# Performance work log

Hardware: AMD Instinct MI355X
Metric: run time of the kernel (lower is better)

## Reference

```python
import jax, jax.numpy as jnp
import numpy as np

HEADS = 8  # head_count from init_kwargs

def _conv1x1(x, W, b):
    # x: [B,C,H,W], W: [Cout,Cin], b: [Cout] -> [B,Cout,H,W]
    return jnp.einsum('bchw,kc->bkhw', x, W) + b[None, :, None, None]

def setup_inputs() -> dict:
    key = jax.random.key(0)
    ks = jax.random.split(key, 9)
    B, C, H, W = 16, 128, 128, 128
    KC, VC = 128, 128
    s = 0.05
    return {
        'x':  jax.random.normal(ks[0], (B, C, H, W), dtype=jnp.float32),
        'Wk': jax.random.normal(ks[1], (KC, C), dtype=jnp.float32) * s,
        'bk': jnp.zeros((KC,), dtype=jnp.float32),
        'Wq': jax.random.normal(ks[2], (KC, C), dtype=jnp.float32) * s,
        'bq': jnp.zeros((KC,), dtype=jnp.float32),
        'Wv': jax.random.normal(ks[3], (VC, C), dtype=jnp.float32) * s,
        'bv': jnp.zeros((VC,), dtype=jnp.float32),
        'Wr': jax.random.normal(ks[4], (C, VC), dtype=jnp.float32) * s,
        'br': jnp.zeros((C,), dtype=jnp.float32),
    }

def reference(x, Wk, bk, Wq, bq, Wv, bv, Wr, br):
    B, C, H, W = x.shape
    N = H * W
    KC, VC = Wk.shape[0], Wv.shape[0]
    dk, dv = KC // HEADS, VC // HEADS

    keys = _conv1x1(x, Wk, bk).reshape(B, HEADS, dk, N)
    queries = _conv1x1(x, Wq, bq).reshape(B, HEADS, dk, N)
    values = _conv1x1(x, Wv, bv).reshape(B, HEADS, dv, N)

    k = jax.nn.softmax(keys, axis=-1)      # softmax over spatial positions
    q = jax.nn.softmax(queries, axis=2)    # softmax over per-head key channels

    # context: [B,h,dk,dv] = sum_n k[b,h,k,n] * v[b,h,v,n]
    context = jnp.einsum('bhkn,bhvn->bhkv', k, values)
    # attended: [B,h,dv,N] = context^T @ q
    attended = jnp.einsum('bhkv,bhkn->bhvn', context, q)
    aggregated = attended.reshape(B, VC, H, W)

    reprojected = _conv1x1(aggregated, Wr, br)
    return reprojected + x
```

## Files before the change

kernel.cpp:

```cpp
#include <hip/hip_runtime.h>
#include <hip/hip_bf16.h>

#define BATCH 16
#define CH    128
#define NPIX  16384
#define NHEAD 8

typedef __attribute__((ext_vector_type(8))) short bf16x8;
typedef __attribute__((ext_vector_type(4))) float f32x4;

__device__ __forceinline__ short f2b(float f) {
    union { float f; unsigned u; } v; v.f = f;
    unsigned r = v.u + 0x7fffu + ((v.u >> 16) & 1u);
    return (short)(r >> 16);
}
__device__ __forceinline__ float b2f(ushort u) {
    union { unsigned u; float f; } v; v.u = ((unsigned)u) << 16; return v.f;
}

__device__ __forceinline__ int xswz(int p, int c) {
    const int v = ((p >> 2) & 15) ^ ((p & 3) << 2);
    return (p * CH + c) ^ (v << 3);
}

__global__ __launch_bounds__(256)
void k1_context(const float* __restrict__ x,
                const float* __restrict__ Wk, const float* __restrict__ bk,
                const float* __restrict__ Wv, const float* __restrict__ bv,
                float* __restrict__ Sp, float* __restrict__ Zp)
{
    __shared__ __align__(16) ushort xlds[64 * CH];

    const int tid  = threadIdx.x;
    const int w    = tid >> 6;
    const int lane = tid & 63;
    const int lo   = lane & 15;
    const int hi   = lane >> 4;

    const int b     = blockIdx.x >> 6;
    const int chunk = blockIdx.x & 63;
    const float* xb = x + (size_t)b * CH * NPIX;

    const int pc = tid >> 4;
    const int pL = tid & 15;

    float4 pf[8];
    {
        const int p0 = chunk * 256;
        #pragma unroll
        for (int i = 0; i < 8; ++i)
            pf[i] = *(const float4*)(xb + (size_t)(pc + 16*i) * NPIX + p0 + pL * 4);
    }

    bf16x8 wkf[2][4], wvf[2][4];
    #pragma unroll
    for (int ct = 0; ct < 2; ++ct) {
        const int row = 32*w + ct*16 + lo;
        #pragma unroll
        for (int ks = 0; ks < 4; ++ks) {
            const int c0 = ks*32 + hi*8;
            const float4 k0 = *(const float4*)(Wk + row*CH + c0);
            const float4 k1 = *(const float4*)(Wk + row*CH + c0 + 4);
            const float4 v0 = *(const float4*)(Wv + row*CH + c0);
            const float4 v1 = *(const float4*)(Wv + row*CH + c0 + 4);
            bf16x8 fk, fv;
            fk[0]=f2b(k0.x); fk[1]=f2b(k0.y); fk[2]=f2b(k0.z); fk[3]=f2b(k0.w);
            fk[4]=f2b(k1.x); fk[5]=f2b(k1.y); fk[6]=f2b(k1.z); fk[7]=f2b(k1.w);
            fv[0]=f2b(v0.x); fv[1]=f2b(v0.y); fv[2]=f2b(v0.z); fv[3]=f2b(v0.w);
            fv[4]=f2b(v1.x); fv[5]=f2b(v1.y); fv[6]=f2b(v1.z); fv[7]=f2b(v1.w);
            wkf[ct][ks] = fk; wvf[ct][ks] = fv;
        }
    }
    float bkv[2], bvv[2];
    #pragma unroll
    for (int ct = 0; ct < 2; ++ct) {
        bkv[ct] = bk[32*w + ct*16 + lo];
        bvv[ct] = bv[32*w + ct*16 + lo];
    }

    const f32x4 zero4 = {0.f, 0.f, 0.f, 0.f};
    f32x4 sacc[2] = {zero4, zero4};
    float zacc[2] = {0.f, 0.f};

    #pragma unroll
    for (int sub = 0; sub < 4; ++sub) {
        #pragma unroll
        for (int i = 0; i < 8; ++i) {
            const int c = pc + 16*i;
            #pragma unroll
            for (int kk = 0; kk < 4; ++kk)
                xlds[xswz(pL*4 + kk, c)] = (ushort)f2b(((const float*)&pf[i])[kk]);
        }
        __syncthreads();

        if (sub < 3) {
            const int pn = chunk*256 + (sub+1)*64;
            #pragma unroll
            for (int i = 0; i < 8; ++i)
                pf[i] = *(const float4*)(xb + (size_t)(pc + 16*i) * NPIX + pn + pL * 4);
        }

        #pragma unroll
        for (int ct = 0; ct < 2; ++ct) {
            f32x4 dk_[4], dv_[4];
            #pragma unroll
            for (int pt = 0; pt < 4; ++pt) { dk_[pt] = zero4; dv_[pt] = zero4; }
            #pragma unroll
            for (int ks = 0; ks < 4; ++ks) {
                #pragma unroll
                for (int pt = 0; pt < 4; ++pt) {
                    const bf16x8 xa = *(const bf16x8*)&xlds[xswz(pt*16 + lo, ks*32 + hi*8)];
                    dk_[pt] = __builtin_amdgcn_mfma_f32_16x16x32_bf16(xa, wkf[ct][ks], dk_[pt], 0, 0, 0);
                    dv_[pt] = __builtin_amdgcn_mfma_f32_16x16x32_bf16(xa, wvf[ct][ks], dv_[pt], 0, 0, 0);
                }
            }
            bf16x8 ef[2], vf[2];
            #pragma unroll
            for (int pt = 0; pt < 4; ++pt) {
                #pragma unroll
                for (int r = 0; r < 4; ++r) {
                    float e = __expf(dk_[pt][r] + bkv[ct]);
                    zacc[ct] += e;
                    ef[pt >> 1][(pt & 1)*4 + r] = f2b(e);
                    vf[pt >> 1][(pt & 1)*4 + r] = f2b(dv_[pt][r] + bvv[ct]);
                }
            }
            #pragma unroll
            for (int kg = 0; kg < 2; ++kg)
                sacc[ct] = __builtin_amdgcn_mfma_f32_16x16x32_bf16(ef[kg], vf[kg], sacc[ct], 0, 0, 0);
        }
        __syncthreads();
    }

    float* sp = Sp + (size_t)(b*64 + chunk) * 2048;
    #pragma unroll
    for (int ct = 0; ct < 2; ++ct)
        #pragma unroll
        for (int r = 0; r < 4; ++r)
            sp[(2*w + ct)*256 + (hi*4 + r)*16 + lo] = sacc[ct][r];

    #pragma unroll
    for (int ct = 0; ct < 2; ++ct) {
        float z = zacc[ct];
        z += __shfl_xor(z, 16, 64);
        z += __shfl_xor(z, 32, 64);
        if (hi == 0)
            Zp[(size_t)(b*64 + chunk) * 128 + 32*w + ct*16 + lo] = z;
    }
}

__global__ __launch_bounds__(256)
void k1b_reduce(const float* __restrict__ Sp, const float* __restrict__ Zp,
                float* __restrict__ Sg, float* __restrict__ Zg)
{
    const int b = blockIdx.y;
    const int j = blockIdx.x * 256 + threadIdx.x;
    if (j < 2048) {
        const float* p = Sp + (size_t)b * 64 * 2048 + j;
        float a = 0.f;
        #pragma unroll 8
        for (int c = 0; c < 64; ++c) a += p[(size_t)c * 2048];
        Sg[b*2048 + j] = a;
    } else if (j < 2176) {
        const int k = j - 2048;
        const float* p = Zp + (size_t)b * 64 * 128 + k;
        float a = 0.f;
        #pragma unroll 8
        for (int c = 0; c < 64; ++c) a += p[(size_t)c * 128];
        Zg[b*128 + k] = a;
    }
}

__global__ __launch_bounds__(256)
void k15_meff(const float* __restrict__ Sg, const float* __restrict__ Zg,
              const float* __restrict__ Wr, ushort* __restrict__ Meffh)
{
    const int b   = blockIdx.x >> 6;
    const int idx = (blockIdx.x & 63) * 256 + threadIdx.x;
    const int c   = idx >> 7;
    const int kcg = idx & 127;
    const int h   = kcg >> 4;
    const int kc  = kcg & 15;
    const float* sp = Sg + (size_t)b*2048 + h*256 + kc*16;
    const float* wr = Wr + (size_t)c * CH + h*16;
    float acc = 0.f;
    #pragma unroll
    for (int v4i = 0; v4i < 4; ++v4i) {
        const float4 sv = *(const float4*)(sp + v4i*4);
        const float4 wv = *(const float4*)(wr + v4i*4);
        acc += sv.x*wv.x + sv.y*wv.y + sv.z*wv.z + sv.w*wv.w;
    }
    Meffh[((size_t)b*CH + c)*CH + kcg] = (ushort)f2b(acc / Zg[b*128 + kcg]);
}

__global__ __launch_bounds__(256)
void k2_out(const float* __restrict__ x,
            const float* __restrict__ Wq, const float* __restrict__ bq,
            const ushort* __restrict__ Meffh, const float* __restrict__ br,
            float* __restrict__ out)
{
    __shared__ __align__(16) ushort xlds[64 * CH];
    __shared__ __align__(16) ushort qlds[64 * CH];
    __shared__ __align__(16) ushort ylds[64 * CH];

    const int tid  = threadIdx.x;
    const int w    = tid >> 6;
    const int lane = tid & 63;
    const int lo   = lane & 15;
    const int hi   = lane >> 4;

    const int b     = blockIdx.x >> 6;
    const int chunk = blockIdx.x & 63;
    const size_t xbase = (size_t)b * CH * NPIX;
    const float* xb = x + xbase;
    float* outb = out + xbase;

    const int pc = tid >> 4;
    const int pL = tid & 15;

    float4 pf[8];
    {
        const int p0 = chunk * 256;
        #pragma unroll
        for (int i = 0; i < 8; ++i)
            pf[i] = *(const float4*)(xb + (size_t)(pc + 16*i) * NPIX + p0 + pL * 4);
    }

    bf16x8 wqf[2][4], mf[2][4];
    #pragma unroll
    for (int ct = 0; ct < 2; ++ct) {
        const int row = 32*w + ct*16 + lo;
        #pragma unroll
        for (int ks = 0; ks < 4; ++ks) {
            const int c0 = ks*32 + hi*8;
            const float4 q0 = *(const float4*)(Wq + row*CH + c0);
            const float4 q1 = *(const float4*)(Wq + row*CH + c0 + 4);
            bf16x8 fq;
            fq[0]=f2b(q0.x); fq[1]=f2b(q0.y); fq[2]=f2b(q0.z); fq[3]=f2b(q0.w);
            fq[4]=f2b(q1.x); fq[5]=f2b(q1.y); fq[6]=f2b(q1.z); fq[7]=f2b(q1.w);
            wqf[ct][ks] = fq;
            mf[ct][ks] = *(const bf16x8*)(Meffh + ((size_t)b*CH + row)*CH + c0);
        }
    }
    float bqv[2];
    #pragma unroll
    for (int ct = 0; ct < 2; ++ct) bqv[ct] = bq[32*w + ct*16 + lo];
    float brv2[8];
    #pragma unroll
    for (int i = 0; i < 8; ++i) brv2[i] = br[pc + 16*i];

    const f32x4 zero4 = {0.f, 0.f, 0.f, 0.f};

    #pragma unroll
    for (int sub = 0; sub < 4; ++sub) {
        const int p0 = chunk*256 + sub*64;

        #pragma unroll
        for (int i = 0; i < 8; ++i) {
            const int c = pc + 16*i;
            #pragma unroll
            for (int kk = 0; kk < 4; ++kk)
                xlds[xswz(pL*4 + kk, c)] = (ushort)f2b(((const float*)&pf[i])[kk]);
        }
        __syncthreads();

        if (sub < 3) {
            const int pn = chunk*256 + (sub+1)*64;
            #pragma unroll
            for (int i = 0; i < 8; ++i)
                pf[i] = *(const float4*)(xb + (size_t)(pc + 16*i) * NPIX + pn + pL * 4);
        }

        f32x4 dq[2][4];
        #pragma unroll
        for (int ct = 0; ct < 2; ++ct)
            #pragma unroll
            for (int pt = 0; pt < 4; ++pt) dq[ct][pt] = zero4;
        #pragma unroll
        for (int ks = 0; ks < 4; ++ks) {
            #pragma unroll
            for (int pt = 0; pt < 4; ++pt) {
                const bf16x8 xa = *(const bf16x8*)&xlds[xswz(pt*16 + lo, ks*32 + hi*8)];
                #pragma unroll
                for (int ct = 0; ct < 2; ++ct)
                    dq[ct][pt] = __builtin_amdgcn_mfma_f32_16x16x32_bf16(xa, wqf[ct][ks], dq[ct][pt], 0, 0, 0);
            }
        }

        #pragma unroll
        for (int ct = 0; ct < 2; ++ct) {
            const int qc = 32*w + ct*16 + lo;
            #pragma unroll
            for (int pt = 0; pt < 4; ++pt) {
                #pragma unroll
                for (int r = 0; r < 4; ++r) {
                    const float e = __expf(dq[ct][pt][r] + bqv[ct]);
                    float s = e;
                    s += __shfl_xor(s, 1, 64);
                    s += __shfl_xor(s, 2, 64);
                    s += __shfl_xor(s, 4, 64);
                    s += __shfl_xor(s, 8, 64);
                    const float q = e / s;
                    const int pos = pt*16 + hi*4 + r;
                    const int sidx = (pos*CH + qc) ^ ((pos & 7) << 3);
                    qlds[sidx] = (ushort)f2b(q);
                }
            }
        }
        __syncthreads();

        f32x4 d2[2][4];
        #pragma unroll
        for (int ct = 0; ct < 2; ++ct)
            #pragma unroll
            for (int pt = 0; pt < 4; ++pt) d2[ct][pt] = zero4;
        #pragma unroll
        for (int ks = 0; ks < 4; ++ks) {
            #pragma unroll
            for (int pt = 0; pt < 4; ++pt) {
                const int pos  = pt*16 + lo;
                const int sidx = (pos*CH + ks*32 + hi*8) ^ ((pos & 7) << 3);
                const bf16x8 qf = *(const bf16x8*)&qlds[sidx];
                #pragma unroll
                for (int ct = 0; ct < 2; ++ct)
                    d2[ct][pt] = __builtin_amdgcn_mfma_f32_16x16x32_bf16(mf[ct][ks], qf, d2[ct][pt], 0, 0, 0);
            }
        }

        #pragma unroll
        for (int ct = 0; ct < 2; ++ct)
            #pragma unroll
            for (int pt = 0; pt < 4; ++pt) {
                #pragma unroll
                for (int r = 0; r < 4; ++r) {
                    const int c = 32*w + ct*16 + hi*4 + r;
                    const int e = c*64 + ((pt*16 + lo) ^ ((c & 7) << 3));
                    ylds[e] = (ushort)f2b(d2[ct][pt][r]);
                }
            }
        __syncthreads();

        #pragma unroll
        for (int i = 0; i < 8; ++i) {
            const int c = pc + 16*i;
            const size_t g = (size_t)c * NPIX + p0 + pL * 4;
            const float4 x4 = *(const float4*)(xb + g);
            const ushort4 y4 = *(const ushort4*)&ylds[c*64 + 4*(pL ^ ((c & 7) << 1))];
            float4 o;
            o.x = b2f(y4.x) + brv2[i] + x4.x;
            o.y = b2f(y4.y) + brv2[i] + x4.y;
            o.z = b2f(y4.z) + brv2[i] + x4.z;
            o.w = b2f(y4.w) + brv2[i] + x4.w;
            *(float4*)(outb + g) = o;
        }
    }
}

extern "C" void kernel_launch(void* const* d_in, const int* in_sizes, int n_in,
                              void* d_out, int out_size, void* d_ws, size_t ws_size,
                              hipStream_t stream)
{
    const float* x  = (const float*)d_in[0];
    const float* Wk = (const float*)d_in[1];
    const float* bk = (const float*)d_in[2];
    const float* Wq = (const float*)d_in[3];
    const float* bq = (const float*)d_in[4];
    const float* Wv = (const float*)d_in[5];
    const float* bv = (const float*)d_in[6];
    const float* Wr = (const float*)d_in[7];
    const float* br = (const float*)d_in[8];
    float* out = (float*)d_out;

    float*  Sp    = (float*)d_ws;
    float*  Zp    = Sp + (size_t)16*64*2048;
    float*  Sg    = Zp + (size_t)16*64*128;
    float*  Zg    = Sg + 32768;
    ushort* Meffh = (ushort*)(Zg + 2048);

    k1_context<<<dim3(BATCH * 64), dim3(256), 0, stream>>>(x, Wk, bk, Wv, bv, Sp, Zp);
    k1b_reduce<<<dim3(9, BATCH),   dim3(256), 0, stream>>>(Sp, Zp, Sg, Zg);
    k15_meff  <<<dim3(BATCH * 64), dim3(256), 0, stream>>>(Sg, Zg, Wr, Meffh);
    k2_out    <<<dim3(BATCH * 64), dim3(256), 0, stream>>>(x, Wq, bq, Meffh, br, out);
}
```

Before: 436.1 us.

## Halve per-block pixel chunk, double-buffer LDS, write output directly without staging

Doubles the grid for the context and output kernels by giving each block 128 pixels instead of 256, which raises parallelism and latency hiding. The context kernel uses a double-buffered LDS tile and drops the trailing barrier. The output kernel removes the ylds staging buffer and its barrier, writing results directly with the residual read back from the bf16 x tile in LDS. This uses a bf16-rounded residual and scalar strided stores, and it also swaps the division for a reciprocal. The cost is more partial sums for the reduce kernel and less-coalesced output stores.

```diff
diff --git a/kernel.cpp b/kernel.cpp
--- a/kernel.cpp
+++ b/kernel.cpp
@@ -29,7 +29,7 @@
                 const float* __restrict__ Wv, const float* __restrict__ bv,
                 float* __restrict__ Sp, float* __restrict__ Zp)
 {
-    __shared__ __align__(16) ushort xlds[64 * CH];
+    __shared__ __align__(16) ushort xlds[2][64 * CH];
 
     const int tid  = threadIdx.x;
     const int w    = tid >> 6;
@@ -37,8 +37,8 @@
     const int lo   = lane & 15;
     const int hi   = lane >> 4;
 
-    const int b     = blockIdx.x >> 6;
-    const int chunk = blockIdx.x & 63;
+    const int b     = blockIdx.x >> 7;
+    const int chunk = blockIdx.x & 127;
     const float* xb = x + (size_t)b * CH * NPIX;
 
     const int pc = tid >> 4;
@@ -46,7 +46,7 @@
 
     float4 pf[8];
     {
-        const int p0 = chunk * 256;
+        const int p0 = chunk * 128;
         #pragma unroll
         for (int i = 0; i < 8; ++i)
             pf[i] = *(const float4*)(xb + (size_t)(pc + 16*i) * NPIX + p0 + pL * 4);
@@ -83,18 +83,21 @@
     float zacc[2] = {0.f, 0.f};
 
     #pragma unroll
-    for (int sub = 0; sub < 4; ++sub) {
-        #pragma unroll
-        for (int i = 0; i < 8; ++i) {
-            const int c = pc + 16*i;
-            #pragma unroll
-            for (int kk = 0; kk < 4; ++kk)
-                xlds[xswz(pL*4 + kk, c)] = (ushort)f2b(((const float*)&pf[i])[kk]);
+    for (int sub = 0; sub < 2; ++sub) {
+        ushort* buf = &xlds[sub][0];
+        if (sub == 0) {
+            #pragma unroll
+            for (int i = 0; i < 8; ++i) {
+                const int c = pc + 16*i;
+                #pragma unroll
+                for (int kk = 0; kk < 4; ++kk)
+                    buf[xswz(pL*4 + kk, c)] = (ushort)f2b(((const float*)&pf[i])[kk]);
+            }
         }
         __syncthreads();
 
-        if (sub < 3) {
-            const int pn = chunk*256 + (sub+1)*64;
+        if (sub == 0) {
+            const int pn = chunk*128 + 64;
             #pragma unroll
             for (int i = 0; i < 8; ++i)
                 pf[i] = *(const float4*)(xb + (size_t)(pc + 16*i) * NPIX + pn + pL * 4);
@@ -109,7 +112,7 @@
             for (int ks = 0; ks < 4; ++ks) {
                 #pragma unroll
                 for (int pt = 0; pt < 4; ++pt) {
-                    const bf16x8 xa = *(const bf16x8*)&xlds[xswz(pt*16 + lo, ks*32 + hi*8)];
+                    const bf16x8 xa = *(const bf16x8*)&buf[xswz(pt*16 + lo, ks*32 + hi*8)];
                     dk_[pt] = __builtin_amdgcn_mfma_f32_16x16x32_bf16(xa, wkf[ct][ks], dk_[pt], 0, 0, 0);
                     dv_[pt] = __builtin_amdgcn_mfma_f32_16x16x32_bf16(xa, wvf[ct][ks], dv_[pt], 0, 0, 0);
                 }
@@ -129,10 +132,20 @@
             for (int kg = 0; kg < 2; ++kg)
                 sacc[ct] = __builtin_amdgcn_mfma_f32_16x16x32_bf16(ef[kg], vf[kg], sacc[ct], 0, 0, 0);
         }
-        __syncthreads();
-    }
-
-    float* sp = Sp + (size_t)(b*64 + chunk) * 2048;
+
+        if (sub == 0) {
+            ushort* nb = &xlds[1][0];
+            #pragma unroll
+            for (int i = 0; i < 8; ++i) {
+                const int c = pc + 16*i;
+                #pragma unroll
+                for (int kk = 0; kk < 4; ++kk)
+                    nb[xswz(pL*4 + kk, c)] = (ushort)f2b(((const float*)&pf[i])[kk]);
+            }
+        }
+    }
+
+    float* sp = Sp + (size_t)(b*128 + chunk) * 2048;
     #pragma unroll
     for (int ct = 0; ct < 2; ++ct)
         #pragma unroll
@@ -145,7 +158,7 @@
         z += __shfl_xor(z, 16, 64);
         z += __shfl_xor(z, 32, 64);
         if (hi == 0)
-            Zp[(size_t)(b*64 + chunk) * 128 + 32*w + ct*16 + lo] = z;
+            Zp[(size_t)(b*128 + chunk) * 128 + 32*w + ct*16 + lo] = z;
     }
 }
 
@@ -156,17 +169,17 @@
     const int b = blockIdx.y;
     const int j = blockIdx.x * 256 + threadIdx.x;
     if (j < 2048) {
-        const float* p = Sp + (size_t)b * 64 * 2048 + j;
+        const float* p = Sp + (size_t)b * 128 * 2048 + j;
         float a = 0.f;
         #pragma unroll 8
-        for (int c = 0; c < 64; ++c) a += p[(size_t)c * 2048];
+        for (int c = 0; c < 128; ++c) a += p[(size_t)c * 2048];
         Sg[b*2048 + j] = a;
     } else if (j < 2176) {
         const int k = j - 2048;
-        const float* p = Zp + (size_t)b * 64 * 128 + k;
+        const float* p = Zp + (size_t)b * 128 * 128 + k;
         float a = 0.f;
         #pragma unroll 8
-        for (int c = 0; c < 64; ++c) a += p[(size_t)c * 128];
+        for (int c = 0; c < 128; ++c) a += p[(size_t)c * 128];
         Zg[b*128 + k] = a;
     }
 }
@@ -201,7 +214,6 @@
 {
     __shared__ __align__(16) ushort xlds[64 * CH];
     __shared__ __align__(16) ushort qlds[64 * CH];
-    __shared__ __align__(16) ushort ylds[64 * CH];
 
     const int tid  = threadIdx.x;
     const int w    = tid >> 6;
@@ -209,8 +221,8 @@
     const int lo   = lane & 15;
     const int hi   = lane >> 4;
 
-    const int b     = blockIdx.x >> 6;
-    const int chunk = blockIdx.x & 63;
+    const int b     = blockIdx.x >> 7;
+    const int chunk = blockIdx.x & 127;
     const size_t xbase = (size_t)b * CH * NPIX;
     const float* xb = x + xbase;
     float* outb = out + xbase;
@@ -220,7 +232,7 @@
 
     float4 pf[8];
     {
-        const int p0 = chunk * 256;
+        const int p0 = chunk * 128;
         #pragma unroll
         for (int i = 0; i < 8; ++i)
             pf[i] = *(const float4*)(xb + (size_t)(pc + 16*i) * NPIX + p0 + pL * 4);
@@ -245,15 +257,17 @@
     float bqv[2];
     #pragma unroll
     for (int ct = 0; ct < 2; ++ct) bqv[ct] = bq[32*w + ct*16 + lo];
-    float brv2[8];
-    #pragma unroll
-    for (int i = 0; i < 8; ++i) brv2[i] = br[pc + 16*i];
+    float brv[2][4];
+    #pragma unroll
+    for (int ct = 0; ct < 2; ++ct)
+        #pragma unroll
+        for (int r = 0; r < 4; ++r) brv[ct][r] = br[32*w + ct*16 + hi*4 + r];
 
     const f32x4 zero4 = {0.f, 0.f, 0.f, 0.f};
 
     #pragma unroll
-    for (int sub = 0; sub < 4; ++sub) {
-        const int p0 = chunk*256 + sub*64;
+    for (int sub = 0; sub < 2; ++sub) {
+        const int p0 = chunk*128 + sub*64;
 
         #pragma unroll
         for (int i = 0; i < 8; ++i) {
@@ -264,8 +278,8 @@
         }
         __syncthreads();
 
-        if (sub < 3) {
-            const int pn = chunk*256 + (sub+1)*64;
+        if (sub == 0) {
+            const int pn = chunk*128 + 64;
             #pragma unroll
             for (int i = 0; i < 8; ++i)
                 pf[i] = *(const float4*)(xb + (size_t)(pc + 16*i) * NPIX + pn + pL * 4);
@@ -300,7 +314,7 @@
                     s += __shfl_xor(s, 2, 64);
                     s += __shfl_xor(s, 4, 64);
                     s += __shfl_xor(s, 8, 64);
-                    const float q = e / s;
+                    const float q = e * __builtin_amdgcn_rcpf(s);
                     const int pos = pt*16 + hi*4 + r;
                     const int sidx = (pos*CH + qc) ^ ((pos & 7) << 3);
                     qlds[sidx] = (ushort)f2b(q);
@@ -331,28 +345,17 @@
         for (int ct = 0; ct < 2; ++ct)
             #pragma unroll
             for (int pt = 0; pt < 4; ++pt) {
+                const int n   = p0 + pt*16 + lo;
+                const int pos = pt*16 + lo;
                 #pragma unroll
                 for (int r = 0; r < 4; ++r) {
-                    const int c = 32*w + ct*16 + hi*4 + r;
-                    const int e = c*64 + ((pt*16 + lo) ^ ((c & 7) << 3));
-                    ylds[e] = (ushort)f2b(d2[ct][pt][r]);
+                    const int cc = 32*w + ct*16 + hi*4 + r;
+                    outb[(size_t)cc * NPIX + n] =
+                        d2[ct][pt][r] + brv[ct][r] + b2f(xlds[xswz(pos, cc)]);
                 }
             }
-        __syncthreads();
-
-        #pragma unroll
-        for (int i = 0; i < 8; ++i) {
-            const int c = pc + 16*i;
-            const size_t g = (size_t)c * NPIX + p0 + pL * 4;
-            const float4 x4 = *(const float4*)(xb + g);
-            const ushort4 y4 = *(const ushort4*)&ylds[c*64 + 4*(pL ^ ((c & 7) << 1))];
-            float4 o;
-            o.x = b2f(y4.x) + brv2[i] + x4.x;
-            o.y = b2f(y4.y) + brv2[i] + x4.y;
-            o.z = b2f(y4.z) + brv2[i] + x4.z;
-            o.w = b2f(y4.w) + brv2[i] + x4.w;
-            *(float4*)(outb + g) = o;
-        }
+
+        if (sub == 0) __syncthreads();
     }
 }
 
@@ -372,13 +375,13 @@
     float* out = (float*)d_out;
 
     float*  Sp    = (float*)d_ws;
-    float*  Zp    = Sp + (size_t)16*64*2048;
-    float*  Sg    = Zp + (size_t)16*64*128;
+    float*  Zp    = Sp + (size_t)16*128*2048;
+    float*  Sg    = Zp + (size_t)16*128*128;
     float*  Zg    = Sg + 32768;
     ushort* Meffh = (ushort*)(Zg + 2048);
 
-    k1_context<<<dim3(BATCH * 64), dim3(256), 0, stream>>>(x, Wk, bk, Wv, bv, Sp, Zp);
-    k1b_reduce<<<dim3(9, BATCH),   dim3(256), 0, stream>>>(Sp, Zp, Sg, Zg);
-    k15_meff  <<<dim3(BATCH * 64), dim3(256), 0, stream>>>(Sg, Zg, Wr, Meffh);
-    k2_out    <<<dim3(BATCH * 64), dim3(256), 0, stream>>>(x, Wq, bq, Meffh, br, out);
-}
+    k1_context<<<dim3(BATCH * 128), dim3(256), 0, stream>>>(x, Wk, bk, Wv, bv, Sp, Zp);
+    k1b_reduce<<<dim3(9, BATCH),    dim3(256), 0, stream>>>(Sp, Zp, Sg, Zg);
+    k15_meff  <<<dim3(BATCH * 64),  dim3(256), 0, stream>>>(Sg, Zg, Wr, Meffh);
+    k2_out    <<<dim3(BATCH * 128), dim3(256), 0, stream>>>(x, Wq, bq, Meffh, br, out);
+}
```

After: 372.8 us. -14.5%, faster.
